# Optimization experiments

Hardware: AMD Instinct MI355X
Metric: run time of the kernel (lower is better)

## Reference

```python
import jax, jax.numpy as jnp
import numpy as np

N_NODES = 50000
N_EDGES = 800000
D_IN = 64
D_HID = 64
D_OUT = 16


def setup_inputs() -> dict:
    key = jax.random.key(0)
    ks = jax.random.split(key, 20)
    features = jax.random.normal(ks[0], (N_NODES, D_IN), dtype=jnp.float32)
    src = jax.random.randint(ks[1], (N_EDGES,), 0, N_NODES)
    dst = jax.random.randint(ks[2], (N_EDGES,), 0, N_NODES)

    def lin(k, din, dout):
        bound = 1.0 / np.sqrt(din)
        k1, k2 = jax.random.split(k)
        W = jax.random.uniform(k1, (din, dout), jnp.float32, -bound, bound)
        b = jax.random.uniform(k2, (dout,), jnp.float32, -bound, bound)
        return W, b

    W0a, b0a = lin(ks[3], D_IN, D_HID)
    W0b, b0b = lin(ks[4], D_HID, D_HID)
    W1a, b1a = lin(ks[5], D_HID, D_HID)
    W1b, b1b = lin(ks[6], D_HID, D_HID)
    W2a, b2a = lin(ks[7], D_HID, D_HID)
    W2b, b2b = lin(ks[8], D_HID, D_HID)
    Wout, bout = lin(ks[9], D_HID, D_OUT)
    return {
        "features": features, "src": src, "dst": dst,
        "W0a": W0a, "b0a": b0a, "W0b": W0b, "b0b": b0b,
        "W1a": W1a, "b1a": b1a, "W1b": W1b, "b1b": b1b,
        "W2a": W2a, "b2a": b2a, "W2b": W2b, "b2b": b2b,
        "Wout": Wout, "bout": bout,
    }


def reference(features, src, dst,
              W0a, b0a, W0b, b0b,
              W1a, b1a, W1b, b1b,
              W2a, b2a, W2b, b2b,
              Wout, bout):
    N = features.shape[0]

    def gin_layer(h, Wa, ba, Wb, bb):
        # GINConv 'sum': gather source features along edges, scatter-sum to dst
        agg = jax.ops.segment_sum(h[src], dst, num_segments=N)  # [N, D]
        r = h + agg  # (1 + eps) * h + agg with eps = 0 (DGL default)
        # ApplyNodeFunc MLP: Linear -> ReLU -> Linear
        return jax.nn.relu(r @ Wa + ba) @ Wb + bb

    h = gin_layer(features, W0a, b0a, W0b, b0b)
    h = gin_layer(h, W1a, b1a, W1b, b1b)
    h = gin_layer(h, W2a, b2a, W2b, b2b)
    # dgl.mean_nodes over the single graph -> [1, D_HID]
    hg = jnp.mean(h, axis=0, keepdims=True)
    return hg @ Wout + bout  # [1, D_OUT]
```

## Files before the change

kernel.cpp:

```cpp
#include <hip/hip_runtime.h>
#include <hip/hip_bf16.h>


#define NNODES 50000
#define NEDGES 800000
#define DDIM   64
#define DOUT   16

#define CHUNK  4096
#define NB1    196
#define NBUCK  196
#define NB64   782
#define CVTB   1024

#define KCAP   1408

typedef unsigned int uint;
typedef unsigned short ushort;
typedef __attribute__((ext_vector_type(8))) short bf16x8;
typedef __attribute__((ext_vector_type(4))) float f32x4;
typedef __attribute__((ext_vector_type(2))) float f32x2;

#define LSTR 72

static __device__ __forceinline__ uint f2bf(float f) {
    uint u = __float_as_uint(f);
    return (u + 0x7fffu + ((u >> 16) & 1u)) >> 16;
}
static __device__ __forceinline__ float bf_lo(uint u) { return __uint_as_float(u << 16); }
static __device__ __forceinline__ float bf_hi(uint u) { return __uint_as_float(u & 0xffff0000u); }

#define ACC4(vv) do { f32x2 u_;                                   \
    u_.x = bf_lo((vv).x); u_.y = bf_hi((vv).x); c0 += u_;         \
    u_.x = bf_lo((vv).y); u_.y = bf_hi((vv).y); c1 += u_;         \
    u_.x = bf_lo((vv).z); u_.y = bf_hi((vv).z); c2 += u_;         \
    u_.x = bf_lo((vv).w); u_.y = bf_hi((vv).w); c3 += u_; } while (0)

#define ACCP(wv) do {                                                     \
    c0 += __builtin_amdgcn_cvt_pk_f32_fp8((int)(wv).x, false);            \
    c1 += __builtin_amdgcn_cvt_pk_f32_fp8((int)(wv).x, true);             \
    c2 += __builtin_amdgcn_cvt_pk_f32_fp8((int)(wv).y, false);            \
    c3 += __builtin_amdgcn_cvt_pk_f32_fp8((int)(wv).y, true);             \
} while (0)


__global__ __launch_bounds__(256) void s1_kernel(const int* __restrict__ src,
                                                 const int* __restrict__ dst,
                                                 uint* __restrict__ key,
                                                 int* __restrict__ gh,
                                                 const float4* __restrict__ fin4,
                                                 uint2* __restrict__ hb0_2,
                                                 uint* __restrict__ p0u,
                                                 uint* __restrict__ p1u,
                                                 const float* __restrict__ Wa0,
                                                 const float* __restrict__ Wb0,
                                                 const float* __restrict__ Wa1,
                                                 const float* __restrict__ Wb1,
                                                 const float* __restrict__ Wa2,
                                                 const float* __restrict__ Wb2,
                                                 uint* __restrict__ wWT,
                                                 float* __restrict__ part,
                                                 int* __restrict__ ticket) {
    __shared__ int h[NBUCK];
    int blk = blockIdx.x;
    int t = threadIdx.x;
    if (blk < NB1) {
        for (int i = t; i < NBUCK; i += 256) h[i] = 0;
        __syncthreads();
        int base = blk * CHUNK;
        int end = base + CHUNK < NEDGES ? base + CHUNK : NEDGES;
        for (int i = base + t; i < end; i += 256) {
            int d = dst[i];
            key[i] = ((uint)d << 16) | (uint)src[i];
            atomicAdd(&h[d >> 8], 1);
        }
        __syncthreads();
        for (int i = t; i < NBUCK; i += 256) gh[blk * NBUCK + i] = h[i];
        return;
    }
    int m = blk - NB1;
    if (m < CVTB) {
        for (int i = m * 256 + t; i < (NNODES + 1) * 16; i += CVTB * 256) {
            uint2 hb; uint pk = 0u;
            if (i < NNODES * 16) {
                float4 v = fin4[i];
                hb.x = f2bf(v.x) | (f2bf(v.y) << 16);
                hb.y = f2bf(v.z) | (f2bf(v.w) << 16);
                int w0 = __builtin_amdgcn_cvt_pk_fp8_f32(v.x, v.y, 0, false);
                w0 = __builtin_amdgcn_cvt_pk_fp8_f32(v.z, v.w, w0, true);
                pk = (uint)w0;
            } else { hb.x = 0u; hb.y = 0u; }
            hb0_2[i] = hb;
            p0u[i] = pk;
        }
        return;
    }
    m -= CVTB;
    if (m < 6) {
        const float* Wm = (m == 0) ? Wa0 : (m == 1) ? Wb0 : (m == 2) ? Wa1
                        : (m == 3) ? Wb1 : (m == 4) ? Wa2 : Wb2;
        for (int o = t; o < 2048; o += 256) {
            int nn = o >> 5, kk = o & 31;
            wWT[m * 2048 + o] = f2bf(Wm[(2 * kk) * 64 + nn]) |
                                (f2bf(Wm[(2 * kk + 1) * 64 + nn]) << 16);
        }
        return;
    }
    if (t < 64) part[t] = 0.f;
    if (t == 64) *ticket = 0;
    if (t >= 128 && t < 144) p1u[NNODES * 16 + (t - 128)] = 0u;
}


__global__ __launch_bounds__(256) void sort_offsets_a_kernel(const int* __restrict__ gh,
                                                             int* __restrict__ offraw,
                                                             int* __restrict__ tot) {
    __shared__ int s[256];
    int b = blockIdx.x;
    int i = threadIdx.x;
    int v = (i < NB1) ? gh[i * NBUCK + b] : 0;
    s[i] = v;
    __syncthreads();
    for (int off = 1; off < 256; off <<= 1) {
        int add = (i >= off) ? s[i - off] : 0;
        __syncthreads();
        s[i] += add;
        __syncthreads();
    }
    if (i < NB1) offraw[i * NBUCK + b] = s[i] - v;
    if (i == 255) tot[b] = s[255];
}


__global__ __launch_bounds__(256) void sort_scatter1_kernel(const uint* __restrict__ key,
                                                            const int* __restrict__ offraw,
                                                            const int* __restrict__ tot,
                                                            uint* __restrict__ out) {
    __shared__ int s[256];
    __shared__ int cur[NBUCK];
    int blk = blockIdx.x;
    int t = threadIdx.x;
    int v = (t < NBUCK) ? tot[t] : 0;
    s[t] = v;
    __syncthreads();
    for (int off = 1; off < 256; off <<= 1) {
        int add = (t >= off) ? s[t - off] : 0;
        __syncthreads();
        s[t] += add;
        __syncthreads();
    }
    if (t < NBUCK) cur[t] = (s[t] - v) + offraw[blk * NBUCK + t];
    __syncthreads();
    int base = blk * CHUNK;
    int end = base + CHUNK < NEDGES ? base + CHUNK : NEDGES;
    for (int j = base + t; j < end; j += 256) {
        uint k = key[j];
        int pos = atomicAdd(&cur[k >> 24], 1);
        out[pos] = k;
    }
}


__global__ __launch_bounds__(256) void sort_bucket_kernel(const uint* __restrict__ in,
                                                          const int* __restrict__ tot,
                                                          int* __restrict__ rowptr,
                                                          uint* __restrict__ out) {
    __shared__ int s[256];
    __shared__ int hh[256];
    __shared__ int cur[256];
    __shared__ int slo[2];
    int blk = blockIdx.x;
    int t = threadIdx.x;
    int v = (t < NBUCK) ? tot[t] : 0;
    s[t] = v;
    __syncthreads();
    for (int off = 1; off < 256; off <<= 1) {
        int add = (t >= off) ? s[t - off] : 0;
        __syncthreads();
        s[t] += add;
        __syncthreads();
    }
    if (t == blk) { slo[0] = s[t] - v; slo[1] = s[t]; }
    hh[t] = 0;
    __syncthreads();
    int lo = slo[0], hi = slo[1];
    for (int i = lo + t; i < hi; i += 256)
        atomicAdd(&hh[(in[i] >> 16) & 255], 1);
    __syncthreads();
    int hv = hh[t];
    s[t] = hv;
    __syncthreads();
    for (int off = 1; off < 256; off <<= 1) {
        int add = (t >= off) ? s[t - off] : 0;
        __syncthreads();
        s[t] += add;
        __syncthreads();
    }
    cur[t] = lo + s[t] - hv;
    __syncthreads();
    int node = (blk << 8) + t;
    if (node < NNODES) rowptr[node] = cur[t];
    if (blk == NBUCK - 1 && t == 0) rowptr[NNODES] = NEDGES;
    __syncthreads();
    for (int i = lo + t; i < hi; i += 256) {
        uint k = in[i];
        int pos = atomicAdd(&cur[(k >> 16) & 255], 1);
        out[pos] = k;
    }
}


__global__ __launch_bounds__(512, 4) void gin_layer_kernel(const uint4* __restrict__ h128,
                                                           const uint2* __restrict__ pin,
                                                           const int* __restrict__ rowptr,
                                                           const uint* __restrict__ skey,
                                                           const uint4* __restrict__ wa4,
                                                           const uint4* __restrict__ wb4,
                                                           const float* __restrict__ ba,
                                                           const float* __restrict__ bb,
                                                           uint4* __restrict__ out128,
                                                           uint2* __restrict__ pout,
                                                           float* __restrict__ part,
                                                           int* __restrict__ ticket,
                                                           const float* __restrict__ Wout,
                                                           const float* __restrict__ bout,
                                                           float* __restrict__ out, int n) {
    __shared__ ushort sW1[64 * LSTR];
    __shared__ ushort sW2[64 * LSTR];
    __shared__ ushort sX[64 * LSTR];
    __shared__ float sba[64], sbb[64];
    __shared__ ushort sSrc[KCAP + 16];
    __shared__ int sRP[65];
    __shared__ float pool[256];
    __shared__ int lastFlag;

    int t = threadIdx.x;
    int node0 = blockIdx.x * 64;

    for (int i = t; i < 512; i += 512) {
        int nn = i >> 3, k8 = i & 7;
        *(uint4*)&sW1[nn * LSTR + k8 * 8] = wa4[nn * 8 + k8];
        *(uint4*)&sW2[nn * LSTR + k8 * 8] = wb4[nn * 8 + k8];
    }
    if (t < 64) { sba[t] = ba[t]; sbb[t] = bb[t]; }
    if (t >= 64 && t < 129) {
        int idx = node0 + (t - 64);
        sRP[t - 64] = rowptr[idx < n ? idx : n];
    }
    int eBase = rowptr[node0];
    int vEnd = node0 + 64 < n ? node0 + 64 : n;
    int nE = rowptr[vEnd] - eBase;
    int nS = nE < KCAP ? nE : KCAP;
    for (int i = t; i < nS; i += 512) sSrc[i] = (ushort)skey[eBase + i];
    __syncthreads();

    int lane = t & 63;
    int w = t >> 6;
    int g = lane >> 3;
    uint p = (uint)(lane & 7);

    {
        int row = w * 8 + g;
        int v = node0 + row;
        if (v < n) {
            f32x2 c0 = {0.f, 0.f}, c1 = {0.f, 0.f}, c2 = {0.f, 0.f}, c3 = {0.f, 0.f};
            uint4 su = h128[(uint)v * 8u + p];
            ACC4(su);
            int e0r = sRP[row], e1r = sRP[row + 1];
            for (int e = e0r; e < e1r; e += 16) {
                int eo = e - eBase;
                uint k0 = sSrc[eo + 0];
                uint k1  = (e + 1  < e1r) ? (uint)sSrc[eo + 1]  : 50000u;
                uint k2  = (e + 2  < e1r) ? (uint)sSrc[eo + 2]  : 50000u;
                uint k3  = (e + 3  < e1r) ? (uint)sSrc[eo + 3]  : 50000u;
                uint k4  = (e + 4  < e1r) ? (uint)sSrc[eo + 4]  : 50000u;
                uint k5  = (e + 5  < e1r) ? (uint)sSrc[eo + 5]  : 50000u;
                uint k6  = (e + 6  < e1r) ? (uint)sSrc[eo + 6]  : 50000u;
                uint k7  = (e + 7  < e1r) ? (uint)sSrc[eo + 7]  : 50000u;
                uint k8  = (e + 8  < e1r) ? (uint)sSrc[eo + 8]  : 50000u;
                uint k9  = (e + 9  < e1r) ? (uint)sSrc[eo + 9]  : 50000u;
                uint k10 = (e + 10 < e1r) ? (uint)sSrc[eo + 10] : 50000u;
                uint k11 = (e + 11 < e1r) ? (uint)sSrc[eo + 11] : 50000u;
                uint k12 = (e + 12 < e1r) ? (uint)sSrc[eo + 12] : 50000u;
                uint k13 = (e + 13 < e1r) ? (uint)sSrc[eo + 13] : 50000u;
                uint k14 = (e + 14 < e1r) ? (uint)sSrc[eo + 14] : 50000u;
                uint k15 = (e + 15 < e1r) ? (uint)sSrc[eo + 15] : 50000u;
                uint2 v0  = pin[k0  * 8u + p];
                uint2 v1  = pin[k1  * 8u + p];
                uint2 v2  = pin[k2  * 8u + p];
                uint2 v3  = pin[k3  * 8u + p];
                uint2 v4  = pin[k4  * 8u + p];
                uint2 v5  = pin[k5  * 8u + p];
                uint2 v6  = pin[k6  * 8u + p];
                uint2 v7  = pin[k7  * 8u + p];
                uint2 v8  = pin[k8  * 8u + p];
                uint2 v9  = pin[k9  * 8u + p];
                uint2 v10 = pin[k10 * 8u + p];
                uint2 v11 = pin[k11 * 8u + p];
                uint2 v12 = pin[k12 * 8u + p];
                uint2 v13 = pin[k13 * 8u + p];
                uint2 v14 = pin[k14 * 8u + p];
                uint2 v15 = pin[k15 * 8u + p];
                ACCP(v0); ACCP(v1); ACCP(v2); ACCP(v3);
                ACCP(v4); ACCP(v5); ACCP(v6); ACCP(v7);
                ACCP(v8); ACCP(v9); ACCP(v10); ACCP(v11);
                ACCP(v12); ACCP(v13); ACCP(v14); ACCP(v15);
            }
            uint4 o;
            o.x = f2bf(c0.x) | (f2bf(c0.y) << 16);
            o.y = f2bf(c1.x) | (f2bf(c1.y) << 16);
            o.z = f2bf(c2.x) | (f2bf(c2.y) << 16);
            o.w = f2bf(c3.x) | (f2bf(c3.y) << 16);
            *(uint4*)&sX[row * LSTR + (int)p * 8] = o;
        }
    }
    __syncthreads();

    int mc = lane & 15;
    int quad = lane >> 4;
    int m0 = w * 16;
    float csum[4] = {0.f, 0.f, 0.f, 0.f};

    if (w < 4) {
        bf16x8 xa0 = *(const bf16x8*)&sX[(m0 + mc) * LSTR + quad * 8];
        bf16x8 xa1 = *(const bf16x8*)&sX[(m0 + mc) * LSTR + 32 + quad * 8];
        ushort hreg[16];
#pragma unroll
        for (int c = 0; c < 4; c++) {
            bf16x8 b0 = *(const bf16x8*)&sW1[(c * 16 + mc) * LSTR + quad * 8];
            bf16x8 b1 = *(const bf16x8*)&sW1[(c * 16 + mc) * LSTR + 32 + quad * 8];
            f32x4 acc = {0.f, 0.f, 0.f, 0.f};
            acc = __builtin_amdgcn_mfma_f32_16x16x32_bf16(xa0, b0, acc, 0, 0, 0);
            acc = __builtin_amdgcn_mfma_f32_16x16x32_bf16(xa1, b1, acc, 0, 0, 0);
            int col = c * 16 + mc;
            float bias = sba[col];
#pragma unroll
            for (int r = 0; r < 4; r++)
                hreg[c * 4 + r] = (ushort)f2bf(fmaxf(acc[r] + bias, 0.f));
        }
#pragma unroll
        for (int c = 0; c < 4; c++) {
            int col = c * 16 + mc;
#pragma unroll
            for (int r = 0; r < 4; r++)
                sX[(m0 + quad * 4 + r) * LSTR + col] = hreg[c * 4 + r];
        }

        bool rok[4];
#pragma unroll
        for (int r = 0; r < 4; r++) rok[r] = (node0 + m0 + quad * 4 + r) < n;

        bf16x8 ha0 = *(const bf16x8*)&sX[(m0 + mc) * LSTR + quad * 8];
        bf16x8 ha1 = *(const bf16x8*)&sX[(m0 + mc) * LSTR + 32 + quad * 8];
#pragma unroll
        for (int c = 0; c < 4; c++) {
            bf16x8 b0 = *(const bf16x8*)&sW2[(c * 16 + mc) * LSTR + quad * 8];
            bf16x8 b1 = *(const bf16x8*)&sW2[(c * 16 + mc) * LSTR + 32 + quad * 8];
            f32x4 acc = {0.f, 0.f, 0.f, 0.f};
            acc = __builtin_amdgcn_mfma_f32_16x16x32_bf16(ha0, b0, acc, 0, 0, 0);
            acc = __builtin_amdgcn_mfma_f32_16x16x32_bf16(ha1, b1, acc, 0, 0, 0);
            int col = c * 16 + mc;
            float bias = sbb[col];
#pragma unroll
            for (int r = 0; r < 4; r++) {
                float val = acc[r] + bias;
                hreg[c * 4 + r] = (ushort)f2bf(val);
                csum[c] += rok[r] ? val : 0.f;
            }
        }

        if (out128) {
#pragma unroll
            for (int c = 0; c < 4; c++) {
                int col = c * 16 + mc;
#pragma unroll
                for (int r = 0; r < 4; r++)
                    sX[(m0 + quad * 4 + r) * LSTR + col] = hreg[c * 4 + r];
            }
#pragma unroll
            for (int i = 0; i < 2; i++) {
                int idx = i * 64 + lane;
                int row16 = idx >> 3, q = idx & 7;
                int row = m0 + row16;
                int gr = node0 + row;
                if (gr < n) {
                    uint4 o = *(const uint4*)&sX[row * LSTR + q * 8];
                    out128[(size_t)gr * 8 + q] = o;
                    float f0 = bf_lo(o.x), f1 = bf_hi(o.x);
                    float f2 = bf_lo(o.y), f3 = bf_hi(o.y);
                    float f4 = bf_lo(o.z), f5 = bf_hi(o.z);
                    float f6 = bf_lo(o.w), f7 = bf_hi(o.w);
                    int w0 = __builtin_amdgcn_cvt_pk_fp8_f32(f0, f1, 0, false);
                    w0 = __builtin_amdgcn_cvt_pk_fp8_f32(f2, f3, w0, true);
                    int w1 = __builtin_amdgcn_cvt_pk_fp8_f32(f4, f5, 0, false);
                    w1 = __builtin_amdgcn_cvt_pk_fp8_f32(f6, f7, w1, true);
                    uint2 pk; pk.x = (uint)w0; pk.y = (uint)w1;
                    pout[(size_t)gr * 8 + q] = pk;
                }
            }
        }
    }

    if (part) {
        if (w < 4) {
#pragma unroll
            for (int c = 0; c < 4; c++) {
                csum[c] += __shfl_xor(csum[c], 16);
                csum[c] += __shfl_xor(csum[c], 32);
            }
            if (quad == 0) {
#pragma unroll
                for (int c = 0; c < 4; c++) pool[w * 64 + c * 16 + mc] = csum[c];
            }
        }
        __syncthreads();
        if (t < 64) {
            float s4 = pool[t] + pool[64 + t] + pool[128 + t] + pool[192 + t];
            atomicAdd(&part[t], s4);
        }
        __syncthreads();
        if (t == 0) {
            __threadfence();
            int old = atomicAdd(ticket, 1);
            lastFlag = (old == NB64 - 1) ? 1 : 0;
        }
        __syncthreads();
        if (lastFlag) {
            if (t < 64)
                pool[t] = __hip_atomic_load(&part[t], __ATOMIC_RELAXED,
                                            __HIP_MEMORY_SCOPE_AGENT) * (1.0f / (float)NNODES);
            __syncthreads();
            if (t < DOUT) {
                float o = bout[t];
                for (int d = 0; d < DDIM; d++) o += pool[d] * Wout[d * DOUT + t];
                out[t] = o;
            }
        }
    }
}


extern "C" void kernel_launch(void* const* d_in, const int* in_sizes, int n_in,
                              void* d_out, int out_size, void* d_ws, size_t ws_size,
                              hipStream_t stream) {
    const float* features = (const float*)d_in[0];
    const int*   src      = (const int*)d_in[1];
    const int*   dst      = (const int*)d_in[2];
    const float* W0a = (const float*)d_in[3];  const float* b0a = (const float*)d_in[4];
    const float* W0b = (const float*)d_in[5];  const float* b0b = (const float*)d_in[6];
    const float* W1a = (const float*)d_in[7];  const float* b1a = (const float*)d_in[8];
    const float* W1b = (const float*)d_in[9];  const float* b1b = (const float*)d_in[10];
    const float* W2a = (const float*)d_in[11]; const float* b2a = (const float*)d_in[12];
    const float* W2b = (const float*)d_in[13]; const float* b2b = (const float*)d_in[14];
    const float* Wout = (const float*)d_in[15]; const float* bout = (const float*)d_in[16];
    float* out = (float*)d_out;

    int* gh     = (int*)d_ws;
    int* offraw = gh + 38416;
    int* tot    = offraw + 38416;
    int* rowptr = tot + 256;
    uint* keybuf = (uint*)(rowptr + 50016);
    uint* buf2   = keybuf + 800000;
    uint* hb0    = buf2 + 800000;
    uint* hb1    = hb0 + (NNODES + 1) * 32;
    uint* p0u    = hb1 + (NNODES + 1) * 32;
    uint* p1u    = p0u + (NNODES + 1) * 16;
    float* part  = (float*)(p1u + (NNODES + 1) * 16);
    int* ticket  = (int*)(part + 64);
    uint* wWT    = (uint*)(ticket + 4);

    s1_kernel<<<NB1 + CVTB + 7, 256, 0, stream>>>(src, dst, keybuf, gh,
                                                  (const float4*)features,
                                                  (uint2*)hb0, p0u, p1u,
                                                  W0a, W0b, W1a, W1b, W2a, W2b,
                                                  wWT, part, ticket);
    sort_offsets_a_kernel<<<NBUCK, 256, 0, stream>>>(gh, offraw, tot);
    sort_scatter1_kernel<<<NB1, 256, 0, stream>>>(keybuf, offraw, tot, buf2);
    sort_bucket_kernel<<<NBUCK, 256, 0, stream>>>(buf2, tot, rowptr, keybuf);

    gin_layer_kernel<<<NB64, 512, 0, stream>>>((const uint4*)hb0, (const uint2*)p0u,
                                               rowptr, keybuf,
                                               (const uint4*)(wWT + 0 * 2048),
                                               (const uint4*)(wWT + 1 * 2048),
                                               b0a, b0b, (uint4*)hb1, (uint2*)p1u,
                                               nullptr, nullptr, nullptr, nullptr, nullptr, NNODES);
    gin_layer_kernel<<<NB64, 512, 0, stream>>>((const uint4*)hb1, (const uint2*)p1u,
                                               rowptr, keybuf,
                                               (const uint4*)(wWT + 2 * 2048),
                                               (const uint4*)(wWT + 3 * 2048),
                                               b1a, b1b, (uint4*)hb0, (uint2*)p0u,
                                               nullptr, nullptr, nullptr, nullptr, nullptr, NNODES);
    gin_layer_kernel<<<NB64, 512, 0, stream>>>((const uint4*)hb0, (const uint2*)p0u,
                                               rowptr, keybuf,
                                               (const uint4*)(wWT + 4 * 2048),
                                               (const uint4*)(wWT + 5 * 2048),
                                               b2a, b2b, nullptr, nullptr,
                                               part, ticket, Wout, bout, out, NNODES);
}
```

Baseline: 191.5 us.

## Process 128 nodes per block with 16-byte fp8 gathers and all waves on MMA

Each block of the GIN layer kernel now covers 128 nodes instead of 64. Four lanes per node each gather 16 bytes of fp8 neighbour features, replacing eight lanes loading 8 bytes each. All eight waves now run the MLP MMA stage on their own 16 rows instead of only four waves, so the block barrier between aggregation and MLP is dropped. The edge-cache capacity and the pooling buffers grow to match. The aim is fewer, wider gather loads, better wave utilisation and less weight staging per node. The risks are higher LDS use per block and a grid of 391 blocks, which may balance worse across CUs than 782.

```diff
diff --git a/kernel.cpp b/kernel.cpp
--- a/kernel.cpp
+++ b/kernel.cpp
@@ -10,10 +10,10 @@
 #define CHUNK  4096
 #define NB1    196
 #define NBUCK  196
-#define NB64   782
+#define NB128  391
 #define CVTB   1024
 
-#define KCAP   1408
+#define KCAP   2688
 
 typedef unsigned int uint;
 typedef unsigned short ushort;
@@ -35,12 +35,21 @@
     u_.x = bf_lo((vv).y); u_.y = bf_hi((vv).y); c1 += u_;         \
     u_.x = bf_lo((vv).z); u_.y = bf_hi((vv).z); c2 += u_;         \
     u_.x = bf_lo((vv).w); u_.y = bf_hi((vv).w); c3 += u_; } while (0)
-
-#define ACCP(wv) do {                                                     \
+#define ACC4H(vv) do { f32x2 u_;                                  \
+    u_.x = bf_lo((vv).x); u_.y = bf_hi((vv).x); c4 += u_;         \
+    u_.x = bf_lo((vv).y); u_.y = bf_hi((vv).y); c5 += u_;         \
+    u_.x = bf_lo((vv).z); u_.y = bf_hi((vv).z); c6 += u_;         \
+    u_.x = bf_lo((vv).w); u_.y = bf_hi((vv).w); c7 += u_; } while (0)
+
+#define ACCQ(wv) do {                                                     \
     c0 += __builtin_amdgcn_cvt_pk_f32_fp8((int)(wv).x, false);            \
     c1 += __builtin_amdgcn_cvt_pk_f32_fp8((int)(wv).x, true);             \
     c2 += __builtin_amdgcn_cvt_pk_f32_fp8((int)(wv).y, false);            \
     c3 += __builtin_amdgcn_cvt_pk_f32_fp8((int)(wv).y, true);             \
+    c4 += __builtin_amdgcn_cvt_pk_f32_fp8((int)(wv).z, false);            \
+    c5 += __builtin_amdgcn_cvt_pk_f32_fp8((int)(wv).z, true);             \
+    c6 += __builtin_amdgcn_cvt_pk_f32_fp8((int)(wv).w, false);            \
+    c7 += __builtin_amdgcn_cvt_pk_f32_fp8((int)(wv).w, true);             \
 } while (0)
 
 
@@ -211,7 +220,7 @@
 
 
 __global__ __launch_bounds__(512, 4) void gin_layer_kernel(const uint4* __restrict__ h128,
-                                                           const uint2* __restrict__ pin,
+                                                           const uint4* __restrict__ pin,
                                                            const int* __restrict__ rowptr,
                                                            const uint* __restrict__ skey,
                                                            const uint4* __restrict__ wa4,
@@ -227,28 +236,28 @@
                                                            float* __restrict__ out, int n) {
     __shared__ ushort sW1[64 * LSTR];
     __shared__ ushort sW2[64 * LSTR];
-    __shared__ ushort sX[64 * LSTR];
+    __shared__ ushort sX[128 * LSTR];
     __shared__ float sba[64], sbb[64];
-    __shared__ ushort sSrc[KCAP + 16];
-    __shared__ int sRP[65];
-    __shared__ float pool[256];
+    __shared__ ushort sSrc[KCAP + 8];
+    __shared__ int sRP[129];
+    __shared__ float pool[512];
     __shared__ int lastFlag;
 
     int t = threadIdx.x;
-    int node0 = blockIdx.x * 64;
-
-    for (int i = t; i < 512; i += 512) {
-        int nn = i >> 3, k8 = i & 7;
+    int node0 = blockIdx.x * 128;
+
+    {
+        int nn = t >> 3, k8 = t & 7;
         *(uint4*)&sW1[nn * LSTR + k8 * 8] = wa4[nn * 8 + k8];
         *(uint4*)&sW2[nn * LSTR + k8 * 8] = wb4[nn * 8 + k8];
     }
     if (t < 64) { sba[t] = ba[t]; sbb[t] = bb[t]; }
-    if (t >= 64 && t < 129) {
+    if (t >= 64 && t < 193) {
         int idx = node0 + (t - 64);
         sRP[t - 64] = rowptr[idx < n ? idx : n];
     }
     int eBase = rowptr[node0];
-    int vEnd = node0 + 64 < n ? node0 + 64 : n;
+    int vEnd = node0 + 128 < n ? node0 + 128 : n;
     int nE = rowptr[vEnd] - eBase;
     int nS = nE < KCAP ? nE : KCAP;
     for (int i = t; i < nS; i += 512) sSrc[i] = (ushort)skey[eBase + i];
@@ -256,72 +265,61 @@
 
     int lane = t & 63;
     int w = t >> 6;
-    int g = lane >> 3;
-    uint p = (uint)(lane & 7);
+    int g = lane >> 2;
+    uint p = (uint)(lane & 3);
+    int m0 = w * 16;
 
     {
-        int row = w * 8 + g;
+        int row = m0 + g;
         int v = node0 + row;
         if (v < n) {
             f32x2 c0 = {0.f, 0.f}, c1 = {0.f, 0.f}, c2 = {0.f, 0.f}, c3 = {0.f, 0.f};
-            uint4 su = h128[(uint)v * 8u + p];
-            ACC4(su);
+            f32x2 c4 = {0.f, 0.f}, c5 = {0.f, 0.f}, c6 = {0.f, 0.f}, c7 = {0.f, 0.f};
+            uint4 su0 = h128[(uint)v * 8u + 2u * p];
+            uint4 su1 = h128[(uint)v * 8u + 2u * p + 1u];
+            ACC4(su0);
+            ACC4H(su1);
             int e0r = sRP[row], e1r = sRP[row + 1];
-            for (int e = e0r; e < e1r; e += 16) {
+            for (int e = e0r; e < e1r; e += 8) {
                 int eo = e - eBase;
                 uint k0 = sSrc[eo + 0];
-                uint k1  = (e + 1  < e1r) ? (uint)sSrc[eo + 1]  : 50000u;
-                uint k2  = (e + 2  < e1r) ? (uint)sSrc[eo + 2]  : 50000u;
-                uint k3  = (e + 3  < e1r) ? (uint)sSrc[eo + 3]  : 50000u;
-                uint k4  = (e + 4  < e1r) ? (uint)sSrc[eo + 4]  : 50000u;
-                uint k5  = (e + 5  < e1r) ? (uint)sSrc[eo + 5]  : 50000u;
-                uint k6  = (e + 6  < e1r) ? (uint)sSrc[eo + 6]  : 50000u;
-                uint k7  = (e + 7  < e1r) ? (uint)sSrc[eo + 7]  : 50000u;
-                uint k8  = (e + 8  < e1r) ? (uint)sSrc[eo + 8]  : 50000u;
-                uint k9  = (e + 9  < e1r) ? (uint)sSrc[eo + 9]  : 50000u;
-                uint k10 = (e + 10 < e1r) ? (uint)sSrc[eo + 10] : 50000u;
-                uint k11 = (e + 11 < e1r) ? (uint)sSrc[eo + 11] : 50000u;
-                uint k12 = (e + 12 < e1r) ? (uint)sSrc[eo + 12] : 50000u;
-                uint k13 = (e + 13 < e1r) ? (uint)sSrc[eo + 13] : 50000u;
-                uint k14 = (e + 14 < e1r) ? (uint)sSrc[eo + 14] : 50000u;
-                uint k15 = (e + 15 < e1r) ? (uint)sSrc[eo + 15] : 50000u;
-                uint2 v0  = pin[k0  * 8u + p];
-                uint2 v1  = pin[k1  * 8u + p];
-                uint2 v2  = pin[k2  * 8u + p];
-                uint2 v3  = pin[k3  * 8u + p];
-                uint2 v4  = pin[k4  * 8u + p];
-                uint2 v5  = pin[k5  * 8u + p];
-                uint2 v6  = pin[k6  * 8u + p];
-                uint2 v7  = pin[k7  * 8u + p];
-                uint2 v8  = pin[k8  * 8u + p];
-                uint2 v9  = pin[k9  * 8u + p];
-                uint2 v10 = pin[k10 * 8u + p];
-                uint2 v11 = pin[k11 * 8u + p];
-                uint2 v12 = pin[k12 * 8u + p];
-                uint2 v13 = pin[k13 * 8u + p];
-                uint2 v14 = pin[k14 * 8u + p];
-                uint2 v15 = pin[k15 * 8u + p];
-                ACCP(v0); ACCP(v1); ACCP(v2); ACCP(v3);
-                ACCP(v4); ACCP(v5); ACCP(v6); ACCP(v7);
-                ACCP(v8); ACCP(v9); ACCP(v10); ACCP(v11);
-                ACCP(v12); ACCP(v13); ACCP(v14); ACCP(v15);
+                uint k1 = (e + 1 < e1r) ? (uint)sSrc[eo + 1] : 50000u;
+                uint k2 = (e + 2 < e1r) ? (uint)sSrc[eo + 2] : 50000u;
+                uint k3 = (e + 3 < e1r) ? (uint)sSrc[eo + 3] : 50000u;
+                uint k4 = (e + 4 < e1r) ? (uint)sSrc[eo + 4] : 50000u;
+                uint k5 = (e + 5 < e1r) ? (uint)sSrc[eo + 5] : 50000u;
+                uint k6 = (e + 6 < e1r) ? (uint)sSrc[eo + 6] : 50000u;
+                uint k7 = (e + 7 < e1r) ? (uint)sSrc[eo + 7] : 50000u;
+                uint4 v0 = pin[k0 * 4u + p];
+                uint4 v1 = pin[k1 * 4u + p];
+                uint4 v2 = pin[k2 * 4u + p];
+                uint4 v3 = pin[k3 * 4u + p];
+                uint4 v4 = pin[k4 * 4u + p];
+                uint4 v5 = pin[k5 * 4u + p];
+                uint4 v6 = pin[k6 * 4u + p];
+                uint4 v7 = pin[k7 * 4u + p];
+                ACCQ(v0); ACCQ(v1); ACCQ(v2); ACCQ(v3);
+                ACCQ(v4); ACCQ(v5); ACCQ(v6); ACCQ(v7);
             }
-            uint4 o;
-            o.x = f2bf(c0.x) | (f2bf(c0.y) << 16);
-            o.y = f2bf(c1.x) | (f2bf(c1.y) << 16);
-            o.z = f2bf(c2.x) | (f2bf(c2.y) << 16);
-            o.w = f2bf(c3.x) | (f2bf(c3.y) << 16);
-            *(uint4*)&sX[row * LSTR + (int)p * 8] = o;
-        }
-    }
-    __syncthreads();
+            uint4 o0, o1;
+            o0.x = f2bf(c0.x) | (f2bf(c0.y) << 16);
+            o0.y = f2bf(c1.x) | (f2bf(c1.y) << 16);
+            o0.z = f2bf(c2.x) | (f2bf(c2.y) << 16);
+            o0.w = f2bf(c3.x) | (f2bf(c3.y) << 16);
+            o1.x = f2bf(c4.x) | (f2bf(c4.y) << 16);
+            o1.y = f2bf(c5.x) | (f2bf(c5.y) << 16);
+            o1.z = f2bf(c6.x) | (f2bf(c6.y) << 16);
+            o1.w = f2bf(c7.x) | (f2bf(c7.y) << 16);
+            *(uint4*)&sX[row * LSTR + (int)p * 16] = o0;
+            *(uint4*)&sX[row * LSTR + (int)p * 16 + 8] = o1;
+        }
+    }
 
     int mc = lane & 15;
     int quad = lane >> 4;
-    int m0 = w * 16;
     float csum[4] = {0.f, 0.f, 0.f, 0.f};
 
-    if (w < 4) {
+    {
         bf16x8 xa0 = *(const bf16x8*)&sX[(m0 + mc) * LSTR + quad * 8];
         bf16x8 xa1 = *(const bf16x8*)&sX[(m0 + mc) * LSTR + 32 + quad * 8];
         ushort hreg[16];
@@ -402,27 +400,27 @@
     }
 
     if (part) {
-        if (w < 4) {
-#pragma unroll
-            for (int c = 0; c < 4; c++) {
-                csum[c] += __shfl_xor(csum[c], 16);
-                csum[c] += __shfl_xor(csum[c], 32);
-            }
-            if (quad == 0) {
-#pragma unroll
-                for (int c = 0; c < 4; c++) pool[w * 64 + c * 16 + mc] = csum[c];
-            }
+#pragma unroll
+        for (int c = 0; c < 4; c++) {
+            csum[c] += __shfl_xor(csum[c], 16);
+            csum[c] += __shfl_xor(csum[c], 32);
+        }
+        if (quad == 0) {
+#pragma unroll
+            for (int c = 0; c < 4; c++) pool[w * 64 + c * 16 + mc] = csum[c];
         }
         __syncthreads();
         if (t < 64) {
-            float s4 = pool[t] + pool[64 + t] + pool[128 + t] + pool[192 + t];
-            atomicAdd(&part[t], s4);
+            float s8 = 0.f;
+#pragma unroll
+            for (int gg = 0; gg < 8; gg++) s8 += pool[gg * 64 + t];
+            atomicAdd(&part[t], s8);
         }
         __syncthreads();
         if (t == 0) {
             __threadfence();
             int old = atomicAdd(ticket, 1);
-            lastFlag = (old == NB64 - 1) ? 1 : 0;
+            lastFlag = (old == NB128 - 1) ? 1 : 0;
         }
         __syncthreads();
         if (lastFlag) {
@@ -478,22 +476,22 @@
     sort_scatter1_kernel<<<NB1, 256, 0, stream>>>(keybuf, offraw, tot, buf2);
     sort_bucket_kernel<<<NBUCK, 256, 0, stream>>>(buf2, tot, rowptr, keybuf);
 
-    gin_layer_kernel<<<NB64, 512, 0, stream>>>((const uint4*)hb0, (const uint2*)p0u,
-                                               rowptr, keybuf,
-                                               (const uint4*)(wWT + 0 * 2048),
-                                               (const uint4*)(wWT + 1 * 2048),
-                                               b0a, b0b, (uint4*)hb1, (uint2*)p1u,
-                                               nullptr, nullptr, nullptr, nullptr, nullptr, NNODES);
-    gin_layer_kernel<<<NB64, 512, 0, stream>>>((const uint4*)hb1, (const uint2*)p1u,
-                                               rowptr, keybuf,
-                                               (const uint4*)(wWT + 2 * 2048),
-                                               (const uint4*)(wWT + 3 * 2048),
-                                               b1a, b1b, (uint4*)hb0, (uint2*)p0u,
-                                               nullptr, nullptr, nullptr, nullptr, nullptr, NNODES);
-    gin_layer_kernel<<<NB64, 512, 0, stream>>>((const uint4*)hb0, (const uint2*)p0u,
-                                               rowptr, keybuf,
-                                               (const uint4*)(wWT + 4 * 2048),
-                                               (const uint4*)(wWT + 5 * 2048),
-                                               b2a, b2b, nullptr, nullptr,
-                                               part, ticket, Wout, bout, out, NNODES);
-}
+    gin_layer_kernel<<<NB128, 512, 0, stream>>>((const uint4*)hb0, (const uint4*)p0u,
+                                                rowptr, keybuf,
+                                                (const uint4*)(wWT + 0 * 2048),
+                                                (const uint4*)(wWT + 1 * 2048),
+                                                b0a, b0b, (uint4*)hb1, (uint2*)p1u,
+                                                nullptr, nullptr, nullptr, nullptr, nullptr, NNODES);
+    gin_layer_kernel<<<NB128, 512, 0, stream>>>((const uint4*)hb1, (const uint4*)p1u,
+                                                rowptr, keybuf,
+                                                (const uint4*)(wWT + 2 * 2048),
+                                                (const uint4*)(wWT + 3 * 2048),
+                                                b1a, b1b, (uint4*)hb0, (uint2*)p0u,
+                                                nullptr, nullptr, nullptr, nullptr, nullptr, NNODES);
+    gin_layer_kernel<<<NB128, 512, 0, stream>>>((const uint4*)hb0, (const uint4*)p0u,
+                                                rowptr, keybuf,
+                                                (const uint4*)(wWT + 4 * 2048),
+                                                (const uint4*)(wWT + 5 * 2048),
+                                                b2a, b2b, nullptr, nullptr,
+                                                part, ticket, Wout, bout, out, NNODES);
+}
```

Result: faster. 174.3 us (-9.0%).
